# Kernel tuning notes

Hardware: AMD Instinct MI355X
Metric: run time of the kernel (lower is better)

## Reference

```python
import math
import jax, jax.numpy as jnp
import numpy as np

BATCH = 2048
LATENT = 64
BETA = 6.0
LOG_2PI = math.log(2.0 * math.pi)


def setup_inputs() -> dict:
    key = jax.random.key(0)
    k1, k2, k3 = jax.random.split(key, 3)
    z = jax.random.normal(k1, (BATCH, LATENT), dtype=jnp.float32)
    z_mean = jax.random.normal(k2, (BATCH, LATENT), dtype=jnp.float32)
    z_logvar = jax.random.normal(k3, (BATCH, LATENT), dtype=jnp.float32)
    return {"z": z, "z_mean": z_mean, "z_logvar": z_logvar}


def _gaussian_log_density(samples, mean, log_var):
    # elementwise Gaussian log-density, broadcasts to [B, B, L]
    inv_sigma = jnp.exp(-log_var)
    tmp = samples - mean
    return -0.5 * (tmp * tmp * inv_sigma + log_var + LOG_2PI)


def _total_correlation(z, z_mean, z_logvar):
    # log q(z_i | x_j) per-dim: [B, B, L]
    log_qz_prob = _gaussian_log_density(z[:, None, :], z_mean[None, :, :], z_logvar[None, :, :])
    # log prod_l (1/B) sum_j q(z_l | x_j)  (constants dropped as in original)
    log_qz_product = jnp.sum(jax.scipy.special.logsumexp(log_qz_prob, axis=1), axis=1)  # [B]
    # log (1/B) sum_j q(z | x_j)
    log_qz = jax.scipy.special.logsumexp(jnp.sum(log_qz_prob, axis=2), axis=1)  # [B]
    return jnp.mean(log_qz - log_qz_product)


def _gaussian_kl(z_mean, z_logvar):
    # standard KL(q(z|x) || N(0, I)), mean over batch
    return 0.5 * jnp.mean(
        jnp.sum(jnp.square(z_mean) + jnp.exp(z_logvar) - z_logvar - 1.0, axis=1)
    )


def reference(z, z_mean, z_logvar):
    kl_loss = _gaussian_kl(z_mean, z_logvar)
    tc = (BETA - 1.0) * _total_correlation(z, z_mean, z_logvar)
    return tc + kl_loss
```

## Files before the change

kernel.cpp:

```cpp
#include <hip/hip_runtime.h>
#include <hip/hip_bf16.h>
#include <math.h>

#define BATCH 2048
#define LATENT 64
#define LOG_2PI 1.8378770664093453f
#define BETA_M1 5.0f
#define LN2 0.69314718055994530942f
#define C2 (-0.72134752044448170368f)

#define OFF_VT   0
#define OFF_TCE  (128*BATCH)
#define OFF_UP   (OFF_TCE + 64*BATCH)
#define OFF_CE   (OFF_UP + 128*BATCH)
#define OFF_KLP  (OFF_CE + BATCH)
#define OFF_RMP  (OFF_KLP + BATCH)
#define OFF_RSP  (OFF_RMP + 2*BATCH)
#define OFF_PART (OFF_RSP + 2*BATCH)
#define OFF_PP   (OFF_PART + 16)

__global__ __launch_bounds__(256) void precompute_kernel(const float* __restrict__ z,
                                                         const float* __restrict__ zm,
                                                         const float* __restrict__ zlv,
                                                         float* __restrict__ ws) {
    __shared__ float Tz[16][65], Tm[16][65], Tlv[16][65];
    __shared__ float CEp[16][16], KLp[16][16];
    int t = threadIdx.x, lane = t & 63, w = t >> 6;
    int j0 = blockIdx.x * 16;

    #pragma unroll
    for (int p = 0; p < 4; ++p) {
        int jr = p * 4 + w;
        int idx = (j0 + jr) * LATENT + lane;
        Tz[jr][lane]  = z[idx];
        Tm[jr][lane]  = zm[idx];
        Tlv[jr][lane] = zlv[idx];
    }
    if (blockIdx.x == 0 && t < 16) ws[OFF_PART + t] = 0.0f;
    __syncthreads();

    int jl = t & 15, lg = t >> 4;
    int j = j0 + jl;
    float ce_acc = 0.0f, kl_acc = 0.0f;
    #pragma unroll
    for (int q = 0; q < 4; ++q) {
        int l = q * 16 + lg;
        float zv = Tz[jl][l];
        float m  = Tm[jl][l];
        float lv = Tlv[jl][l];
        float iv  = __expf(-lv);
        float civ = C2 * iv;
        float miv = m * iv;
        float cmv = C2 * miv;
        float cev = C2 * fmaf(m, miv, lv + LOG_2PI);
        ws[OFF_VT  + (2*l)   * BATCH + j] = civ;
        ws[OFF_VT  + (2*l+1) * BATCH + j] = cmv;
        ws[OFF_TCE + l       * BATCH + j] = cev;
        ws[OFF_UP  + (2*l)   * BATCH + j] = zv * zv;
        ws[OFF_UP  + (2*l+1) * BATCH + j] = -2.0f * zv;
        ce_acc += cev;
        kl_acc += fmaf(m, m, __expf(lv)) - lv - 1.0f;
    }
    CEp[lg][jl] = ce_acc;
    KLp[lg][jl] = kl_acc;
    __syncthreads();
    if (t < 16) {
        float ce = 0.0f, kl = 0.0f;
        #pragma unroll
        for (int g = 0; g < 16; ++g) { ce += CEp[g][t]; kl += KLp[g][t]; }
        ws[OFF_CE  + j0 + t] = ce;
        ws[OFF_KLP + j0 + t] = kl;
    }
}

#define DIMB 512
#define ROWB 512
__global__ __launch_bounds__(256) void main_kernel(float* __restrict__ ws) {
    __shared__ float RMs[8][4], RSs[8][4];
    int bx = blockIdx.x, t = threadIdx.x;

    if (bx < DIMB) {
        int l  = bx >> 3;
        int jc = bx & 7;

        const float* __restrict__ up0 = ws + OFF_UP + (2*l)   * BATCH;
        const float* __restrict__ up1 = ws + OFF_UP + (2*l+1) * BATCH;
        float z2[8], n2[8];
        #pragma unroll
        for (int k = 0; k < 8; ++k) {
            z2[k] = up0[t + 256*k];
            n2[k] = up1[t + 256*k];
        }

        const float* __restrict__ pc = ws + OFF_VT  + (2*l)   * BATCH + jc * 256;
        const float* __restrict__ pm = ws + OFF_VT  + (2*l+1) * BATCH + jc * 256;
        const float* __restrict__ pe = ws + OFF_TCE + l       * BATCH + jc * 256;

        float s[8];
        #pragma unroll
        for (int k = 0; k < 8; ++k) s[k] = 0.0f;

        for (int jj = 0; jj < 256; jj += 8) {
            #pragma unroll
            for (int u = 0; u < 8; ++u) {
                float cc = pc[jj + u];
                float mm = pm[jj + u];
                float ee = pe[jj + u];
                #pragma unroll
                for (int k = 0; k < 8; ++k)
                    s[k] += __builtin_amdgcn_exp2f(fmaf(z2[k], cc, fmaf(n2[k], mm, ee)));
            }
        }

        __hip_bfloat16* pp = (__hip_bfloat16*)(ws + OFF_PP);
        size_t base = ((size_t)(jc * 64 + l)) * BATCH;
        #pragma unroll
        for (int k = 0; k < 8; ++k)
            pp[base + t + 256*k] = __float2bfloat16(s[k]);
    } else {
        int bx2 = bx - DIMB;
        int ib8 = bx2 >> 1, ph = bx2 & 1;
        int i0 = ib8 * 8;
        int jb = ph * 1024 + 4 * t;
        int lane = t & 63, w = t >> 6;

        const float* __restrict__ Vt = ws + OFF_VT;
        const float* __restrict__ Up = ws + OFF_UP;

        float r[8][4];
        #pragma unroll
        for (int i = 0; i < 8; ++i)
            r[i][0] = r[i][1] = r[i][2] = r[i][3] = 0.0f;

        for (int l = 0; l < LATENT; ++l) {
            float4 v0 = *(const float4*)(Vt + (2*l)   * BATCH + jb);
            float4 v1 = *(const float4*)(Vt + (2*l+1) * BATCH + jb);
            const float* __restrict__ u0 = Up + (2*l)   * BATCH + i0;
            const float* __restrict__ u1 = Up + (2*l+1) * BATCH + i0;
            #pragma unroll
            for (int i = 0; i < 8; ++i) {
                float a = u0[i], b = u1[i];
                r[i][0] = fmaf(a, v0.x, fmaf(b, v1.x, r[i][0]));
                r[i][1] = fmaf(a, v0.y, fmaf(b, v1.y, r[i][1]));
                r[i][2] = fmaf(a, v0.z, fmaf(b, v1.z, r[i][2]));
                r[i][3] = fmaf(a, v0.w, fmaf(b, v1.w, r[i][3]));
            }
        }

        float4 ce4 = *(const float4*)(ws + OFF_CE + jb);
        #pragma unroll
        for (int i = 0; i < 8; ++i) {
            float rc0 = r[i][0] + ce4.x, rc1 = r[i][1] + ce4.y;
            float rc2 = r[i][2] + ce4.z, rc3 = r[i][3] + ce4.w;
            float M = fmaxf(fmaxf(rc0, rc1), fmaxf(rc2, rc3));
            float S = __builtin_amdgcn_exp2f(rc0 - M) + __builtin_amdgcn_exp2f(rc1 - M)
                    + __builtin_amdgcn_exp2f(rc2 - M) + __builtin_amdgcn_exp2f(rc3 - M);
            #pragma unroll
            for (int off = 32; off > 0; off >>= 1) {
                float Mo = __shfl_xor(M, off, 64);
                float So = __shfl_xor(S, off, 64);
                float mn = fmaxf(M, Mo);
                S = S * __builtin_amdgcn_exp2f(M - mn) + So * __builtin_amdgcn_exp2f(Mo - mn);
                M = mn;
            }
            if (lane == 0) { RMs[i][w] = M; RSs[i][w] = S; }
        }
        __syncthreads();
        if (t < 8) {
            float M = RMs[t][0], S = RSs[t][0];
            #pragma unroll
            for (int w2 = 1; w2 < 4; ++w2) {
                float Mo = RMs[t][w2], So = RSs[t][w2];
                float mn = fmaxf(M, Mo);
                S = S * __builtin_amdgcn_exp2f(M - mn) + So * __builtin_amdgcn_exp2f(Mo - mn);
                M = mn;
            }
            ws[OFF_RMP + ph * BATCH + i0 + t] = M;
            ws[OFF_RSP + ph * BATCH + i0 + t] = S;
        }
    }
}

__global__ __launch_bounds__(256) void finalize_kernel(float* __restrict__ ws) {
    __shared__ float s_tc[256];
    __shared__ float s_kl[256];
    int t = threadIdx.x;
    int gid = blockIdx.x * 256 + t;

    const __hip_bfloat16* __restrict__ pp = (const __hip_bfloat16*)(ws + OFF_PP);

    float acc = 0.0f, kl = 0.0f;
    #pragma unroll
    for (int k = 0; k < 4; ++k) {
        int f = gid + 32768 * k;
        int l = f >> 11, i = f & 2047;
        float s = 0.0f;
        #pragma unroll
        for (int c = 0; c < 8; ++c)
            s += __bfloat162float(pp[((size_t)(c * 64 + l)) * BATCH + i]);
        acc -= __builtin_amdgcn_logf(s);
    }

    if (gid < BATCH) {
        int i = gid;
        float M0 = ws[OFF_RMP + i], M1 = ws[OFF_RMP + BATCH + i];
        float S0 = ws[OFF_RSP + i], S1 = ws[OFF_RSP + BATCH + i];
        float mn = fmaxf(M0, M1);
        acc += mn + __builtin_amdgcn_logf(
            S0 * __builtin_amdgcn_exp2f(M0 - mn) + S1 * __builtin_amdgcn_exp2f(M1 - mn));
        kl = ws[OFF_KLP + i];
    }

    s_tc[t] = acc; s_kl[t] = kl;
    __syncthreads();
    for (int s = 128; s > 0; s >>= 1) {
        if (t < s) { s_tc[t] += s_tc[t + s]; s_kl[t] += s_kl[t + s]; }
        __syncthreads();
    }
    if (t == 0) {
        atomicAdd(&ws[OFF_PART + 0], s_tc[0]);
        atomicAdd(&ws[OFF_PART + 1], s_kl[0]);
    }
}

__global__ void assemble_kernel(const float* __restrict__ ws,
                                float* __restrict__ out) {
    if (threadIdx.x == 0) {
        float tc = ws[OFF_PART + 0];
        float kl = ws[OFF_PART + 1];
        out[0] = BETA_M1 * (LN2 * tc / (float)BATCH) + 0.5f * (kl / (float)BATCH);
    }
}

extern "C" void kernel_launch(void* const* d_in, const int* in_sizes, int n_in,
                              void* d_out, int out_size, void* d_ws, size_t ws_size,
                              hipStream_t stream) {
    const float* z        = (const float*)d_in[0];
    const float* z_mean   = (const float*)d_in[1];
    const float* z_logvar = (const float*)d_in[2];
    float* out = (float*)d_out;
    float* ws  = (float*)d_ws;

    precompute_kernel<<<128, 256, 0, stream>>>(z, z_mean, z_logvar, ws);
    main_kernel<<<DIMB + ROWB, 256, 0, stream>>>(ws);
    finalize_kernel<<<128, 256, 0, stream>>>(ws);
    assemble_kernel<<<1, 64, 0, stream>>>(ws, out);
}
```

Before: 118.6 us.

## Split work into 2048 blocks each doing a dim slice and row slice; atomic partial sums

Main kernel now launches 2048 blocks. Each block handles a 64-wide j chunk of the per-dimension logsumexp, accumulated with fp32 atomics into a zeroed buffer instead of bf16 partials. Each block also handles a 256-wide j chunk of the row logsumexp, with the U coefficients staged in shared memory. Alternating the order of the two parts across block groups mixes exp-heavy and FMA-heavy work per CU. The assemble kernel is folded into finalize with a last-block counter. This adds atomic traffic and more partial merges, and finalize now reads 8 partials per row.

```diff
diff --git a/kernel.cpp b/kernel.cpp
--- a/kernel.cpp
+++ b/kernel.cpp
@@ -1,5 +1,4 @@
 #include <hip/hip_runtime.h>
-#include <hip/hip_bf16.h>
 #include <math.h>
 
 #define BATCH 2048
@@ -15,9 +14,9 @@
 #define OFF_CE   (OFF_UP + 128*BATCH)
 #define OFF_KLP  (OFF_CE + BATCH)
 #define OFF_RMP  (OFF_KLP + BATCH)
-#define OFF_RSP  (OFF_RMP + 2*BATCH)
-#define OFF_PART (OFF_RSP + 2*BATCH)
-#define OFF_PP   (OFF_PART + 16)
+#define OFF_RSP  (OFF_RMP + 8*BATCH)
+#define OFF_PART (OFF_RSP + 8*BATCH)
+#define OFF_SM   (OFF_PART + 16)
 
 __global__ __launch_bounds__(256) void precompute_kernel(const float* __restrict__ z,
                                                          const float* __restrict__ zm,
@@ -35,6 +34,11 @@
         Tz[jr][lane]  = z[idx];
         Tm[jr][lane]  = zm[idx];
         Tlv[jr][lane] = zlv[idx];
+    }
+    {
+        int gid = blockIdx.x * 256 + t;
+        #pragma unroll
+        for (int k = 0; k < 4; ++k) ws[OFF_SM + gid + 32768 * k] = 0.0f;
     }
     if (blockIdx.x == 0 && t < 16) ws[OFF_PART + t] = 0.0f;
     __syncthreads();
@@ -73,162 +77,161 @@
     }
 }
 
-#define DIMB 512
-#define ROWB 512
-__global__ __launch_bounds__(256) void main_kernel(float* __restrict__ ws) {
+
+__device__ __forceinline__ void dim_part(float* __restrict__ ws, int bx, int t) {
+    int l = bx >> 5, jc = bx & 31;
+    const float* __restrict__ up0 = ws + OFF_UP + (2*l)   * BATCH;
+    const float* __restrict__ up1 = ws + OFF_UP + (2*l+1) * BATCH;
+    float z2[8], n2[8];
+    #pragma unroll
+    for (int k = 0; k < 8; ++k) {
+        z2[k] = up0[t + 256*k];
+        n2[k] = up1[t + 256*k];
+    }
+    const float* __restrict__ pc = ws + OFF_VT  + (2*l)   * BATCH + jc * 64;
+    const float* __restrict__ pm = ws + OFF_VT  + (2*l+1) * BATCH + jc * 64;
+    const float* __restrict__ pe = ws + OFF_TCE + l       * BATCH + jc * 64;
+
+    float s[8];
+    #pragma unroll
+    for (int k = 0; k < 8; ++k) s[k] = 0.0f;
+
+    #pragma unroll 1
+    for (int jj = 0; jj < 64; jj += 8) {
+        #pragma unroll
+        for (int u = 0; u < 8; ++u) {
+            float cc = pc[jj + u];
+            float mm = pm[jj + u];
+            float ee = pe[jj + u];
+            #pragma unroll
+            for (int k = 0; k < 8; ++k)
+                s[k] += __builtin_amdgcn_exp2f(fmaf(z2[k], cc, fmaf(n2[k], mm, ee)));
+        }
+    }
+    #pragma unroll
+    for (int k = 0; k < 8; ++k)
+        atomicAdd(&ws[OFF_SM + l * BATCH + t + 256*k], s[k]);
+}
+
+__device__ __forceinline__ void row_part(float* __restrict__ ws, int bx, int t,
+                                         float* __restrict__ Ups,
+                                         float (*RMs)[4], float (*RSs)[4]) {
+    int ig = bx >> 3, jq = bx & 7;
+    int i0 = ig * 8;
+    int j  = jq * 256 + t;
+
+    #pragma unroll
+    for (int p = 0; p < 4; ++p) {
+        int f = t + 256 * p;
+        Ups[f] = ws[OFF_UP + (f >> 3) * BATCH + i0 + (f & 7)];
+    }
+    __syncthreads();
+
+    float r[8];
+    #pragma unroll
+    for (int i = 0; i < 8; ++i) r[i] = 0.0f;
+
+    const float* __restrict__ Vt = ws + OFF_VT;
+    for (int l = 0; l < LATENT; ++l) {
+        float v0 = Vt[(2*l)   * BATCH + j];
+        float v1 = Vt[(2*l+1) * BATCH + j];
+        const float* __restrict__ ua = Ups + (2*l)   * 8;
+        const float* __restrict__ ub = Ups + (2*l+1) * 8;
+        #pragma unroll
+        for (int i = 0; i < 8; ++i)
+            r[i] = fmaf(ua[i], v0, fmaf(ub[i], v1, r[i]));
+    }
+
+    float ce = ws[OFF_CE + j];
+    int lane = t & 63, w = t >> 6;
+    #pragma unroll
+    for (int i = 0; i < 8; ++i) {
+        float M = r[i] + ce;
+        float S = 1.0f;
+        #pragma unroll
+        for (int off = 32; off > 0; off >>= 1) {
+            float Mo = __shfl_xor(M, off, 64);
+            float So = __shfl_xor(S, off, 64);
+            float mn = fmaxf(M, Mo);
+            S = S * __builtin_amdgcn_exp2f(M - mn) + So * __builtin_amdgcn_exp2f(Mo - mn);
+            M = mn;
+        }
+        if (lane == 0) { RMs[i][w] = M; RSs[i][w] = S; }
+    }
+    __syncthreads();
+    if (t < 8) {
+        float M = RMs[t][0], S = RSs[t][0];
+        #pragma unroll
+        for (int w2 = 1; w2 < 4; ++w2) {
+            float Mo = RMs[t][w2], So = RSs[t][w2];
+            float mn = fmaxf(M, Mo);
+            S = S * __builtin_amdgcn_exp2f(M - mn) + So * __builtin_amdgcn_exp2f(Mo - mn);
+            M = mn;
+        }
+        ws[OFF_RMP + jq * BATCH + i0 + t] = M;
+        ws[OFF_RSP + jq * BATCH + i0 + t] = S;
+    }
+}
+
+__global__ __launch_bounds__(256, 8) void main_kernel(float* __restrict__ ws) {
+    __shared__ float Ups[1024];
     __shared__ float RMs[8][4], RSs[8][4];
     int bx = blockIdx.x, t = threadIdx.x;
-
-    if (bx < DIMB) {
-        int l  = bx >> 3;
-        int jc = bx & 7;
-
-        const float* __restrict__ up0 = ws + OFF_UP + (2*l)   * BATCH;
-        const float* __restrict__ up1 = ws + OFF_UP + (2*l+1) * BATCH;
-        float z2[8], n2[8];
-        #pragma unroll
-        for (int k = 0; k < 8; ++k) {
-            z2[k] = up0[t + 256*k];
-            n2[k] = up1[t + 256*k];
-        }
-
-        const float* __restrict__ pc = ws + OFF_VT  + (2*l)   * BATCH + jc * 256;
-        const float* __restrict__ pm = ws + OFF_VT  + (2*l+1) * BATCH + jc * 256;
-        const float* __restrict__ pe = ws + OFF_TCE + l       * BATCH + jc * 256;
-
-        float s[8];
-        #pragma unroll
-        for (int k = 0; k < 8; ++k) s[k] = 0.0f;
-
-        for (int jj = 0; jj < 256; jj += 8) {
-            #pragma unroll
-            for (int u = 0; u < 8; ++u) {
-                float cc = pc[jj + u];
-                float mm = pm[jj + u];
-                float ee = pe[jj + u];
-                #pragma unroll
-                for (int k = 0; k < 8; ++k)
-                    s[k] += __builtin_amdgcn_exp2f(fmaf(z2[k], cc, fmaf(n2[k], mm, ee)));
-            }
-        }
-
-        __hip_bfloat16* pp = (__hip_bfloat16*)(ws + OFF_PP);
-        size_t base = ((size_t)(jc * 64 + l)) * BATCH;
-        #pragma unroll
-        for (int k = 0; k < 8; ++k)
-            pp[base + t + 256*k] = __float2bfloat16(s[k]);
+    if (((bx >> 8) & 1) == 0) {
+        dim_part(ws, bx, t);
+        row_part(ws, bx, t, Ups, RMs, RSs);
     } else {
-        int bx2 = bx - DIMB;
-        int ib8 = bx2 >> 1, ph = bx2 & 1;
-        int i0 = ib8 * 8;
-        int jb = ph * 1024 + 4 * t;
-        int lane = t & 63, w = t >> 6;
-
-        const float* __restrict__ Vt = ws + OFF_VT;
-        const float* __restrict__ Up = ws + OFF_UP;
-
-        float r[8][4];
-        #pragma unroll
-        for (int i = 0; i < 8; ++i)
-            r[i][0] = r[i][1] = r[i][2] = r[i][3] = 0.0f;
-
-        for (int l = 0; l < LATENT; ++l) {
-            float4 v0 = *(const float4*)(Vt + (2*l)   * BATCH + jb);
-            float4 v1 = *(const float4*)(Vt + (2*l+1) * BATCH + jb);
-            const float* __restrict__ u0 = Up + (2*l)   * BATCH + i0;
-            const float* __restrict__ u1 = Up + (2*l+1) * BATCH + i0;
-            #pragma unroll
-            for (int i = 0; i < 8; ++i) {
-                float a = u0[i], b = u1[i];
-                r[i][0] = fmaf(a, v0.x, fmaf(b, v1.x, r[i][0]));
-                r[i][1] = fmaf(a, v0.y, fmaf(b, v1.y, r[i][1]));
-                r[i][2] = fmaf(a, v0.z, fmaf(b, v1.z, r[i][2]));
-                r[i][3] = fmaf(a, v0.w, fmaf(b, v1.w, r[i][3]));
-            }
-        }
-
-        float4 ce4 = *(const float4*)(ws + OFF_CE + jb);
-        #pragma unroll
-        for (int i = 0; i < 8; ++i) {
-            float rc0 = r[i][0] + ce4.x, rc1 = r[i][1] + ce4.y;
-            float rc2 = r[i][2] + ce4.z, rc3 = r[i][3] + ce4.w;
-            float M = fmaxf(fmaxf(rc0, rc1), fmaxf(rc2, rc3));
-            float S = __builtin_amdgcn_exp2f(rc0 - M) + __builtin_amdgcn_exp2f(rc1 - M)
-                    + __builtin_amdgcn_exp2f(rc2 - M) + __builtin_amdgcn_exp2f(rc3 - M);
-            #pragma unroll
-            for (int off = 32; off > 0; off >>= 1) {
-                float Mo = __shfl_xor(M, off, 64);
-                float So = __shfl_xor(S, off, 64);
-                float mn = fmaxf(M, Mo);
-                S = S * __builtin_amdgcn_exp2f(M - mn) + So * __builtin_amdgcn_exp2f(Mo - mn);
-                M = mn;
-            }
-            if (lane == 0) { RMs[i][w] = M; RSs[i][w] = S; }
-        }
-        __syncthreads();
-        if (t < 8) {
-            float M = RMs[t][0], S = RSs[t][0];
-            #pragma unroll
-            for (int w2 = 1; w2 < 4; ++w2) {
-                float Mo = RMs[t][w2], So = RSs[t][w2];
-                float mn = fmaxf(M, Mo);
-                S = S * __builtin_amdgcn_exp2f(M - mn) + So * __builtin_amdgcn_exp2f(Mo - mn);
-                M = mn;
-            }
-            ws[OFF_RMP + ph * BATCH + i0 + t] = M;
-            ws[OFF_RSP + ph * BATCH + i0 + t] = S;
-        }
-    }
-}
-
-__global__ __launch_bounds__(256) void finalize_kernel(float* __restrict__ ws) {
+        row_part(ws, bx, t, Ups, RMs, RSs);
+        dim_part(ws, bx, t);
+    }
+}
+
+__global__ __launch_bounds__(256) void finalize_kernel(float* __restrict__ ws,
+                                                       float* __restrict__ out) {
     __shared__ float s_tc[256];
     __shared__ float s_kl[256];
     int t = threadIdx.x;
     int gid = blockIdx.x * 256 + t;
 
-    const __hip_bfloat16* __restrict__ pp = (const __hip_bfloat16*)(ws + OFF_PP);
-
     float acc = 0.0f, kl = 0.0f;
     #pragma unroll
     for (int k = 0; k < 4; ++k) {
-        int f = gid + 32768 * k;
-        int l = f >> 11, i = f & 2047;
-        float s = 0.0f;
-        #pragma unroll
-        for (int c = 0; c < 8; ++c)
-            s += __bfloat162float(pp[((size_t)(c * 64 + l)) * BATCH + i]);
+        float s = ws[OFF_SM + gid + 32768 * k];
         acc -= __builtin_amdgcn_logf(s);
     }
 
     if (gid < BATCH) {
         int i = gid;
-        float M0 = ws[OFF_RMP + i], M1 = ws[OFF_RMP + BATCH + i];
-        float S0 = ws[OFF_RSP + i], S1 = ws[OFF_RSP + BATCH + i];
-        float mn = fmaxf(M0, M1);
-        acc += mn + __builtin_amdgcn_logf(
-            S0 * __builtin_amdgcn_exp2f(M0 - mn) + S1 * __builtin_amdgcn_exp2f(M1 - mn));
+        float M = ws[OFF_RMP + i];
+        float S = ws[OFF_RSP + i];
+        #pragma unroll
+        for (int q = 1; q < 8; ++q) {
+            float Mo = ws[OFF_RMP + q * BATCH + i];
+            float So = ws[OFF_RSP + q * BATCH + i];
+            float mn = fmaxf(M, Mo);
+            S = S * __builtin_amdgcn_exp2f(M - mn) + So * __builtin_amdgcn_exp2f(Mo - mn);
+            M = mn;
+        }
+        acc += M + __builtin_amdgcn_logf(S);
         kl = ws[OFF_KLP + i];
     }
 
     s_tc[t] = acc; s_kl[t] = kl;
     __syncthreads();
-    for (int s = 128; s > 0; s >>= 1) {
-        if (t < s) { s_tc[t] += s_tc[t + s]; s_kl[t] += s_kl[t + s]; }
+    for (int s2 = 128; s2 > 0; s2 >>= 1) {
+        if (t < s2) { s_tc[t] += s_tc[t + s2]; s_kl[t] += s_kl[t + s2]; }
         __syncthreads();
     }
     if (t == 0) {
         atomicAdd(&ws[OFF_PART + 0], s_tc[0]);
         atomicAdd(&ws[OFF_PART + 1], s_kl[0]);
-    }
-}
-
-__global__ void assemble_kernel(const float* __restrict__ ws,
-                                float* __restrict__ out) {
-    if (threadIdx.x == 0) {
-        float tc = ws[OFF_PART + 0];
-        float kl = ws[OFF_PART + 1];
-        out[0] = BETA_M1 * (LN2 * tc / (float)BATCH) + 0.5f * (kl / (float)BATCH);
+        __threadfence();
+        unsigned int old = atomicAdd((unsigned int*)(ws + OFF_PART + 2), 1u);
+        if (old == 127u) {
+            float tc  = atomicAdd(&ws[OFF_PART + 0], 0.0f);
+            float kl2 = atomicAdd(&ws[OFF_PART + 1], 0.0f);
+            out[0] = BETA_M1 * (LN2 * tc / (float)BATCH) + 0.5f * (kl2 / (float)BATCH);
+        }
     }
 }
 
@@ -242,7 +245,6 @@
     float* ws  = (float*)d_ws;
 
     precompute_kernel<<<128, 256, 0, stream>>>(z, z_mean, z_logvar, ws);
-    main_kernel<<<DIMB + ROWB, 256, 0, stream>>>(ws);
-    finalize_kernel<<<128, 256, 0, stream>>>(ws);
-    assemble_kernel<<<1, 64, 0, stream>>>(ws, out);
-}
+    main_kernel<<<2048, 256, 0, stream>>>(ws);
+    finalize_kernel<<<128, 256, 0, stream>>>(ws, out);
+}
```

Result: slower. 214.3 us (+80.7%).
